# Kernel optimization log

Hardware: AMD Instinct MI355X
Metric: run time of the kernel (lower is better)

The kernel has to match this reference:

```python
import jax, jax.numpy as jnp
import numpy as np


def setup_inputs() -> dict:
    key = jax.random.key(0)
    k1, k2 = jax.random.split(key)
    B, S, H, D = 4, 2048, 12, 64
    v = jax.random.normal(k1, (B, S, H, D), dtype=jnp.float32)
    # learned per-head positional weights, sorted ascending along last dim
    # (mirrors torch.sort(torch.randn(H, S), dim=-1)[0])
    w = jnp.sort(jax.random.normal(k2, (H, S), dtype=jnp.float32), axis=-1)
    return {"v": v, "w": w}


def reference(v, w):
    # PositionalBias._naive
    # v: [B, S, H, D]; w: [H, S_max]
    B, S, H, D = v.shape
    seq_len = S - 2  # v[:, 1:-1] is the non-special-token span
    w_ = w[:, :seq_len]  # [H, seq_len]
    # _construct_bias builds bias[h, l, j] = w[h, |l - j|] (symmetric Toeplitz)
    pos = jnp.arange(seq_len)
    idx = jnp.abs(pos[:, None] - pos[None, :])  # [seq_len, seq_len]
    bias = w_[:, idx]  # [H, seq_len, seq_len]
    # zero-pad one row/col on each side -> [H, S, S]
    bias = jnp.pad(bias, ((0, 0), (1, 1), (1, 1)))
    # z_pb: [1, S, H]
    z_pb = jnp.sum(bias, axis=-1).T[None, :, :]
    # pbv: [B, S, H, D]
    pbv = jnp.einsum('nlhd,hlj->njhd', v, bias)
    return (pbv, z_pb)
```

## Files before the change

kernel.cpp:

```cpp
#include <hip/hip_runtime.h>
#include <hip/hip_bf16.h>


typedef short short8 __attribute__((ext_vector_type(8)));
typedef float floatx4 __attribute__((ext_vector_type(4)));

#define TL 2280

__device__ __forceinline__ unsigned short f2bf(float f) {
  union { __hip_bfloat16 b; unsigned short u; } cv;
  cv.b = __float2bfloat16(f);
  return cv.u;
}

__global__ __launch_bounds__(256, 3) void fused_kernel(const float* __restrict__ v,
                                                       const float* __restrict__ w,
                                                       float* __restrict__ out) {
  __shared__ __attribute__((aligned(16))) short Tls[8 * TL];

  const int bx  = blockIdx.x;
  const int tid = threadIdx.x;

  if (bx >= 768) {
    const int h = bx - 768;
    float* wv  = (float*)Tls;
    float* pfx = ((float*)Tls) + 2048;
    __shared__ float wsum[4];
    const float* wh = w + (size_t)h * 2048;
    float* zout = out + 6291456;
    for (int i = tid; i < 2048; i += 256) wv[i] = (i < 2046) ? wh[i] : 0.f;
    __syncthreads();
    const int base = tid * 8;
    float run0 = 0.f;
    #pragma unroll
    for (int k = 0; k < 8; ++k) run0 += wv[base + k];
    float x = run0;
    #pragma unroll
    for (int dd = 1; dd < 64; dd <<= 1) {
      float y = __shfl_up(x, dd);
      if ((tid & 63) >= dd) x += y;
    }
    if ((tid & 63) == 63) wsum[tid >> 6] = x;
    __syncthreads();
    const int wid4 = tid >> 6;
    float woff = 0.f;
    #pragma unroll
    for (int u = 0; u < 3; ++u) { float t = wsum[u]; if (u < wid4) woff += t; }
    float pr = x + woff - run0;
    #pragma unroll
    for (int k = 0; k < 8; ++k) { pr += wv[base + k]; pfx[base + k] = pr; }
    __syncthreads();
    for (int i = tid; i < 2046; i += 256) {
      float z = pfx[i] + pfx[2045 - i] - wv[0];
      zout[(size_t)(i + 1) * 12 + h] = z;
    }
    if (tid == 0) { zout[h] = 0.f; zout[(size_t)2047 * 12 + h] = 0.f; }
    return;
  }

  const int slice = bx % 48;
  const int jt    = bx / 48;
  const int ndt = slice & 3;
  const int h   = slice >> 2;
  const int lane = tid & 63, wid = tid >> 6;
  const int lm = lane & 15, quad = lane >> 4;
  const int jb = jt * 128;
  const int d  = wid * 16 + lm;

  const float* vrow = v + (((size_t)ndt * 2048) * 12 + h) * 64 + d;

  float r0[16], rA[16];
  {
    const int lb = quad * 8;
    #pragma unroll
    for (int i = 0; i < 8; ++i) r0[i]     = vrow[(size_t)(lb + i) * 768];
    #pragma unroll
    for (int i = 0; i < 8; ++i) r0[8 + i] = vrow[(size_t)(lb + 32 + i) * 768];
    #pragma unroll
    for (int i = 0; i < 8; ++i) rA[i]     = vrow[(size_t)(64 + lb + i) * 768];
    #pragma unroll
    for (int i = 0; i < 8; ++i) rA[8 + i] = vrow[(size_t)(64 + 32 + lb + i) * 768];
  }

  const float* wh = w + (size_t)h * 2048;
  for (int g = tid; g < 8 * (TL / 8); g += 256) {
    int c  = g / (TL / 8);
    int p8 = (g - c * (TL / 8)) * 8;
    unsigned short buf[8] __attribute__((aligned(16)));
    #pragma unroll
    for (int i = 0; i < 8; ++i) {
      int t = 127 + jb - (p8 + i) - c;
      int a = t < 0 ? -t : t;
      buf[i] = (a <= 2045) ? f2bf(wh[a]) : (unsigned short)0;
    }
    *(short8*)&Tls[c * TL + p8] = *(const short8*)buf;
  }
  __syncthreads();

  const int abase = 127 + quad * 8 - lm;
  auto load_af = [&](int p) -> short8 {
    int p0 = p + abase;
    int c = p0 & 7;
    return *(const short8*)&Tls[c * TL + (p0 - c)];
  };

  auto packB = [&](const float* f, short8& b0, short8& b1) {
    #pragma unroll
    for (int i = 0; i < 8; ++i) {
      b0[i] = (short)f2bf(f[i]);
      b1[i] = (short)f2bf(f[8 + i]);
    }
  };

  short8 afr[10];
  #pragma unroll
  for (int i = 0; i < 10; ++i) afr[i] = load_af((i - 7) * 16);

  short8 bc0, bc1;
  packB(r0, bc0, bc1);
  if (quad == 0) bc0[0] = 0;

  floatx4 acc[8];
  #pragma unroll
  for (int ma = 0; ma < 8; ++ma) acc[ma] = (floatx4){0.f, 0.f, 0.f, 0.f};

  #pragma unroll
  for (int t = 0; t < 32; ++t) {
    float rN[16];
    if (t < 30) {
      const int lb2 = (t + 2) * 64 + quad * 8;
      #pragma unroll
      for (int i = 0; i < 8; ++i) rN[i]     = vrow[(size_t)(lb2 + i) * 768];
      #pragma unroll
      for (int i = 0; i < 8; ++i) rN[8 + i] = vrow[(size_t)(lb2 + 32 + i) * 768];
    }
    short8 na0, na1, na2, na3;
    if (t < 31) {
      const int l0n = t * 64 + 64;
      na0 = load_af(l0n - 16);
      na1 = load_af(l0n);
      na2 = load_af(l0n + 16);
      na3 = load_af(l0n + 32);
    }

    __builtin_amdgcn_s_setprio(1);
    #pragma unroll
    for (int ma = 0; ma < 8; ++ma)
      acc[ma] = __builtin_amdgcn_mfma_f32_16x16x32_bf16(afr[7 - ma], bc0, acc[ma], 0, 0, 0);
    #pragma unroll
    for (int ma = 0; ma < 8; ++ma)
      acc[ma] = __builtin_amdgcn_mfma_f32_16x16x32_bf16(afr[9 - ma], bc1, acc[ma], 0, 0, 0);
    __builtin_amdgcn_s_setprio(0);

    if (t < 31) {
      short8 nb0, nb1;
      packB(rA, nb0, nb1);
      if (t == 30 && quad == 3) nb1[7] = 0;
      bc0 = nb0; bc1 = nb1;
      #pragma unroll
      for (int i = 0; i < 6; ++i) afr[i] = afr[i + 4];
      afr[6] = na0; afr[7] = na1; afr[8] = na2; afr[9] = na3;
      if (t < 30) {
        #pragma unroll
        for (int i = 0; i < 16; ++i) rA[i] = rN[i];
      }
    }
  }

  float* obase = out + (size_t)ndt * 1572864 + (size_t)h * 64 + d;
  #pragma unroll
  for (int ma = 0; ma < 8; ++ma) {
    floatx4 cc = acc[ma];
    #pragma unroll
    for (int r = 0; r < 4; ++r) {
      int j = jb + ma * 16 + quad * 4 + r;
      float val = (j == 0 || j == 2047) ? 0.f : cc[r];
      obase[(size_t)j * 768] = val;
    }
  }
}

extern "C" void kernel_launch(void* const* d_in, const int* in_sizes, int n_in,
                              void* d_out, int out_size, void* d_ws, size_t ws_size,
                              hipStream_t stream) {
  const float* v = (const float*)d_in[0];
  const float* w = (const float*)d_in[1];
  float* out = (float*)d_out;
  fused_kernel<<<dim3(780), 256, 0, stream>>>(v, w, out);
}
```

Measured before the change: 120.8 us.

## Widen j-tile to 256 and split head dim across blocks with 128-thread blocks

```diff
diff --git a/kernel.cpp b/kernel.cpp
--- a/kernel.cpp
+++ b/kernel.cpp
@@ -5,7 +5,7 @@
 typedef short short8 __attribute__((ext_vector_type(8)));
 typedef float floatx4 __attribute__((ext_vector_type(4)));
 
-#define TL 2280
+#define TL 2304
 
 __device__ __forceinline__ unsigned short f2bf(float f) {
   union { __hip_bfloat16 b; unsigned short u; } cv;
@@ -13,7 +13,7 @@
   return cv.u;
 }
 
-__global__ __launch_bounds__(256, 3) void fused_kernel(const float* __restrict__ v,
+__global__ __launch_bounds__(128, 2) void fused_kernel(const float* __restrict__ v,
                                                        const float* __restrict__ w,
                                                        float* __restrict__ out) {
   __shared__ __attribute__((aligned(16))) short Tls[8 * TL];
@@ -25,15 +25,15 @@
     const int h = bx - 768;
     float* wv  = (float*)Tls;
     float* pfx = ((float*)Tls) + 2048;
-    __shared__ float wsum[4];
+    __shared__ float wsum[2];
     const float* wh = w + (size_t)h * 2048;
     float* zout = out + 6291456;
-    for (int i = tid; i < 2048; i += 256) wv[i] = (i < 2046) ? wh[i] : 0.f;
+    for (int i = tid; i < 2048; i += 128) wv[i] = (i < 2046) ? wh[i] : 0.f;
     __syncthreads();
-    const int base = tid * 8;
+    const int base = tid * 16;
     float run0 = 0.f;
     #pragma unroll
-    for (int k = 0; k < 8; ++k) run0 += wv[base + k];
+    for (int k = 0; k < 16; ++k) run0 += wv[base + k];
     float x = run0;
     #pragma unroll
     for (int dd = 1; dd < 64; dd <<= 1) {
@@ -42,15 +42,12 @@
     }
     if ((tid & 63) == 63) wsum[tid >> 6] = x;
     __syncthreads();
-    const int wid4 = tid >> 6;
-    float woff = 0.f;
-    #pragma unroll
-    for (int u = 0; u < 3; ++u) { float t = wsum[u]; if (u < wid4) woff += t; }
+    float woff = (tid >> 6) ? wsum[0] : 0.f;
     float pr = x + woff - run0;
     #pragma unroll
-    for (int k = 0; k < 8; ++k) { pr += wv[base + k]; pfx[base + k] = pr; }
+    for (int k = 0; k < 16; ++k) { pr += wv[base + k]; pfx[base + k] = pr; }
     __syncthreads();
-    for (int i = tid; i < 2046; i += 256) {
+    for (int i = tid; i < 2046; i += 128) {
       float z = pfx[i] + pfx[2045 - i] - wv[0];
       zout[(size_t)(i + 1) * 12 + h] = z;
     }
@@ -59,37 +56,35 @@
   }
 
   const int slice = bx % 48;
-  const int jt    = bx / 48;
+  const int rest  = bx / 48;
+  const int jp    = rest >> 1;
+  const int dh    = rest & 1;
   const int ndt = slice & 3;
   const int h   = slice >> 2;
   const int lane = tid & 63, wid = tid >> 6;
   const int lm = lane & 15, quad = lane >> 4;
-  const int jb = jt * 128;
-  const int d  = wid * 16 + lm;
+  const int jb = jp * 256;
+  const int d  = dh * 32 + wid * 16 + lm;
 
   const float* vrow = v + (((size_t)ndt * 2048) * 12 + h) * 64 + d;
 
-  float r0[16], rA[16];
+  float r0[16];
   {
     const int lb = quad * 8;
     #pragma unroll
     for (int i = 0; i < 8; ++i) r0[i]     = vrow[(size_t)(lb + i) * 768];
     #pragma unroll
     for (int i = 0; i < 8; ++i) r0[8 + i] = vrow[(size_t)(lb + 32 + i) * 768];
-    #pragma unroll
-    for (int i = 0; i < 8; ++i) rA[i]     = vrow[(size_t)(64 + lb + i) * 768];
-    #pragma unroll
-    for (int i = 0; i < 8; ++i) rA[8 + i] = vrow[(size_t)(64 + 32 + lb + i) * 768];
   }
 
   const float* wh = w + (size_t)h * 2048;
-  for (int g = tid; g < 8 * (TL / 8); g += 256) {
+  for (int g = tid; g < 8 * (TL / 8); g += 128) {
     int c  = g / (TL / 8);
     int p8 = (g - c * (TL / 8)) * 8;
     unsigned short buf[8] __attribute__((aligned(16)));
     #pragma unroll
     for (int i = 0; i < 8; ++i) {
-      int t = 127 + jb - (p8 + i) - c;
+      int t = 255 + jb - (p8 + i) - c;
       int a = t < 0 ? -t : t;
       buf[i] = (a <= 2045) ? f2bf(wh[a]) : (unsigned short)0;
     }
@@ -97,9 +92,9 @@
   }
   __syncthreads();
 
-  const int abase = 127 + quad * 8 - lm;
+  const int ABASE = 255 + quad * 8 - lm;
   auto load_af = [&](int p) -> short8 {
-    int p0 = p + abase;
+    int p0 = p + ABASE;
     int c = p0 & 7;
     return *(const short8*)&Tls[c * TL + (p0 - c)];
   };
@@ -112,23 +107,26 @@
     }
   };
 
-  short8 afr[10];
+  short8 afr[18];
   #pragma unroll
-  for (int i = 0; i < 10; ++i) afr[i] = load_af((i - 7) * 16);
+  for (int i = 0; i < 18; ++i) afr[i] = load_af((i - 15) * 16);
 
   short8 bc0, bc1;
   packB(r0, bc0, bc1);
   if (quad == 0) bc0[0] = 0;
 
-  floatx4 acc[8];
+  floatx4 acc0[8], acc1[8];
   #pragma unroll
-  for (int ma = 0; ma < 8; ++ma) acc[ma] = (floatx4){0.f, 0.f, 0.f, 0.f};
+  for (int ma = 0; ma < 8; ++ma) {
+    acc0[ma] = (floatx4){0.f, 0.f, 0.f, 0.f};
+    acc1[ma] = (floatx4){0.f, 0.f, 0.f, 0.f};
+  }
 
-  #pragma unroll
+  #pragma unroll 4
   for (int t = 0; t < 32; ++t) {
     float rN[16];
-    if (t < 30) {
-      const int lb2 = (t + 2) * 64 + quad * 8;
+    if (t < 31) {
+      const int lb2 = (t + 1) * 64 + quad * 8;
       #pragma unroll
       for (int i = 0; i < 8; ++i) rN[i]     = vrow[(size_t)(lb2 + i) * 768];
       #pragma unroll
@@ -146,36 +144,42 @@
     __builtin_amdgcn_s_setprio(1);
     #pragma unroll
     for (int ma = 0; ma < 8; ++ma)
-      acc[ma] = __builtin_amdgcn_mfma_f32_16x16x32_bf16(afr[7 - ma], bc0, acc[ma], 0, 0, 0);
+      acc0[ma] = __builtin_amdgcn_mfma_f32_16x16x32_bf16(afr[15 - ma], bc0, acc0[ma], 0, 0, 0);
     #pragma unroll
     for (int ma = 0; ma < 8; ++ma)
-      acc[ma] = __builtin_amdgcn_mfma_f32_16x16x32_bf16(afr[9 - ma], bc1, acc[ma], 0, 0, 0);
+      acc1[ma] = __builtin_amdgcn_mfma_f32_16x16x32_bf16(afr[7 - ma], bc0, acc1[ma], 0, 0, 0);
+    #pragma unroll
+    for (int ma = 0; ma < 8; ++ma)
+      acc0[ma] = __builtin_amdgcn_mfma_f32_16x16x32_bf16(afr[17 - ma], bc1, acc0[ma], 0, 0, 0);
+    #pragma unroll
+    for (int ma = 0; ma < 8; ++ma)
+      acc1[ma] = __builtin_amdgcn_mfma_f32_16x16x32_bf16(afr[9 - ma], bc1, acc1[ma], 0, 0, 0);
     __builtin_amdgcn_s_setprio(0);
 
     if (t < 31) {
       short8 nb0, nb1;
-      packB(rA, nb0, nb1);
+      packB(rN, nb0, nb1);
       if (t == 30 && quad == 3) nb1[7] = 0;
       bc0 = nb0; bc1 = nb1;
       #pragma unroll
-      for (int i = 0; i < 6; ++i) afr[i] = afr[i + 4];
-      afr[6] = na0; afr[7] = na1; afr[8] = na2; afr[9] = na3;
-      if (t < 30) {
-        #pragma unroll
-        for (int i = 0; i < 16; ++i) rA[i] = rN[i];
-      }
+      for (int i = 0; i < 14; ++i) afr[i] = afr[i + 4];
+      afr[14] = na0; afr[15] = na1; afr[16] = na2; afr[17] = na3;
     }
   }
 
   float* obase = out + (size_t)ndt * 1572864 + (size_t)h * 64 + d;
   #pragma unroll
   for (int ma = 0; ma < 8; ++ma) {
-    floatx4 cc = acc[ma];
+    floatx4 c0 = acc0[ma];
+    floatx4 c1 = acc1[ma];
     #pragma unroll
     for (int r = 0; r < 4; ++r) {
-      int j = jb + ma * 16 + quad * 4 + r;
-      float val = (j == 0 || j == 2047) ? 0.f : cc[r];
-      obase[(size_t)j * 768] = val;
+      int j0 = jb + ma * 16 + quad * 4 + r;
+      int j1 = j0 + 128;
+      float v0 = (j0 == 0) ? 0.f : c0[r];
+      float v1 = (j1 == 2047) ? 0.f : c1[r];
+      obase[(size_t)j0 * 768] = v0;
+      obase[(size_t)j1 * 768] = v1;
     }
   }
 }
@@ -186,5 +190,5 @@
   const float* v = (const float*)d_in[0];
   const float* w = (const float*)d_in[1];
   float* out = (float*)d_out;
-  fused_kernel<<<dim3(780), 256, 0, stream>>>(v, w, out);
+  fused_kernel<<<dim3(780), 128, 0, stream>>>(v, w, out);
 }
```

New measurement: 118.1 us. 2.2% less time.

## Precompute bf16 Toeplitz table in global memory and split into prep and GEMM kernels

Applied to the files above, without the earlier changes.

```diff
diff --git a/kernel.cpp b/kernel.cpp
--- a/kernel.cpp
+++ b/kernel.cpp
@@ -5,7 +5,9 @@
 typedef short short8 __attribute__((ext_vector_type(8)));
 typedef float floatx4 __attribute__((ext_vector_type(4)));
 
-#define TL 2280
+#define QN 4352
+
+__device__ __attribute__((aligned(16))) short g_wt[12 * QN * 8];
 
 __device__ __forceinline__ unsigned short f2bf(float f) {
   union { __hip_bfloat16 b; unsigned short u; } cv;
@@ -13,96 +15,84 @@
   return cv.u;
 }
 
-__global__ __launch_bounds__(256, 3) void fused_kernel(const float* __restrict__ v,
-                                                       const float* __restrict__ w,
-                                                       float* __restrict__ out) {
-  __shared__ __attribute__((aligned(16))) short Tls[8 * TL];
+__global__ __launch_bounds__(256) void prep_kernel(const float* __restrict__ w,
+                                                   float* __restrict__ out) {
+  __shared__ float zls[4096];
+  __shared__ float wsum[4];
 
   const int bx  = blockIdx.x;
   const int tid = threadIdx.x;
 
-  if (bx >= 768) {
-    const int h = bx - 768;
-    float* wv  = (float*)Tls;
-    float* pfx = ((float*)Tls) + 2048;
-    __shared__ float wsum[4];
+  if (bx < 12) {
+    const int h = bx;
     const float* wh = w + (size_t)h * 2048;
-    float* zout = out + 6291456;
-    for (int i = tid; i < 2048; i += 256) wv[i] = (i < 2046) ? wh[i] : 0.f;
-    __syncthreads();
-    const int base = tid * 8;
-    float run0 = 0.f;
-    #pragma unroll
-    for (int k = 0; k < 8; ++k) run0 += wv[base + k];
-    float x = run0;
-    #pragma unroll
-    for (int dd = 1; dd < 64; dd <<= 1) {
-      float y = __shfl_up(x, dd);
-      if ((tid & 63) >= dd) x += y;
+    short* F = g_wt + (size_t)h * QN * 8;
+    for (int q = tid; q < QN; q += 256) {
+      unsigned short buf[8] __attribute__((aligned(16)));
+      #pragma unroll
+      for (int i = 0; i < 8; ++i) {
+        int t = 2174 - q - i;
+        int a = t < 0 ? -t : t;
+        buf[i] = (a <= 2045) ? f2bf(wh[a]) : (unsigned short)0;
+      }
+      *(short8*)&F[(size_t)q * 8] = *(const short8*)buf;
     }
-    if ((tid & 63) == 63) wsum[tid >> 6] = x;
-    __syncthreads();
-    const int wid4 = tid >> 6;
-    float woff = 0.f;
-    #pragma unroll
-    for (int u = 0; u < 3; ++u) { float t = wsum[u]; if (u < wid4) woff += t; }
-    float pr = x + woff - run0;
-    #pragma unroll
-    for (int k = 0; k < 8; ++k) { pr += wv[base + k]; pfx[base + k] = pr; }
-    __syncthreads();
-    for (int i = tid; i < 2046; i += 256) {
-      float z = pfx[i] + pfx[2045 - i] - wv[0];
-      zout[(size_t)(i + 1) * 12 + h] = z;
-    }
-    if (tid == 0) { zout[h] = 0.f; zout[(size_t)2047 * 12 + h] = 0.f; }
     return;
   }
 
-  const int slice = bx % 48;
-  const int jt    = bx / 48;
-  const int ndt = slice & 3;
-  const int h   = slice >> 2;
-  const int lane = tid & 63, wid = tid >> 6;
+  const int h = bx - 12;
+  float* wvv = zls;
+  float* pfx = zls + 2048;
+  const float* wh = w + (size_t)h * 2048;
+  float* zout = out + 6291456;
+  for (int i = tid; i < 2048; i += 256) wvv[i] = (i < 2046) ? wh[i] : 0.f;
+  __syncthreads();
+  const int base = tid * 8;
+  float run0 = 0.f;
+  #pragma unroll
+  for (int k = 0; k < 8; ++k) run0 += wvv[base + k];
+  float x = run0;
+  #pragma unroll
+  for (int dd = 1; dd < 64; dd <<= 1) {
+    float y = __shfl_up(x, dd);
+    if ((tid & 63) >= dd) x += y;
+  }
+  if ((tid & 63) == 63) wsum[tid >> 6] = x;
+  __syncthreads();
+  const int wid4 = tid >> 6;
+  float woff = 0.f;
+  #pragma unroll
+  for (int u = 0; u < 3; ++u) { float t = wsum[u]; if (u < wid4) woff += t; }
+  float pr = x + woff - run0;
+  #pragma unroll
+  for (int k = 0; k < 8; ++k) { pr += wvv[base + k]; pfx[base + k] = pr; }
+  __syncthreads();
+  for (int i = tid; i < 2046; i += 256) {
+    float z = pfx[i] + pfx[2045 - i] - wvv[0];
+    zout[(size_t)(i + 1) * 12 + h] = z;
+  }
+  if (tid == 0) { zout[h] = 0.f; zout[(size_t)2047 * 12 + h] = 0.f; }
+}
+
+__global__ __launch_bounds__(64, 4) void gemm_kernel(const float* __restrict__ v,
+                                                     float* __restrict__ out) {
+  const int bx   = blockIdx.x;
+  const int lane = threadIdx.x;
+
+  const int slice = bx % 192;
+  const int jt    = bx / 192;
+  const int ndq   = slice & 3;
+  const int sl    = slice >> 2;
+  const int n = sl & 3;
+  const int h = sl >> 2;
   const int lm = lane & 15, quad = lane >> 4;
   const int jb = jt * 128;
-  const int d  = wid * 16 + lm;
+  const int d  = ndq * 16 + lm;
 
-  const float* vrow = v + (((size_t)ndt * 2048) * 12 + h) * 64 + d;
+  const float* vrow = v + (((size_t)n * 2048) * 12 + h) * 64 + d;
 
-  float r0[16], rA[16];
-  {
-    const int lb = quad * 8;
-    #pragma unroll
-    for (int i = 0; i < 8; ++i) r0[i]     = vrow[(size_t)(lb + i) * 768];
-    #pragma unroll
-    for (int i = 0; i < 8; ++i) r0[8 + i] = vrow[(size_t)(lb + 32 + i) * 768];
-    #pragma unroll
-    for (int i = 0; i < 8; ++i) rA[i]     = vrow[(size_t)(64 + lb + i) * 768];
-    #pragma unroll
-    for (int i = 0; i < 8; ++i) rA[8 + i] = vrow[(size_t)(64 + 32 + lb + i) * 768];
-  }
-
-  const float* wh = w + (size_t)h * 2048;
-  for (int g = tid; g < 8 * (TL / 8); g += 256) {
-    int c  = g / (TL / 8);
-    int p8 = (g - c * (TL / 8)) * 8;
-    unsigned short buf[8] __attribute__((aligned(16)));
-    #pragma unroll
-    for (int i = 0; i < 8; ++i) {
-      int t = 127 + jb - (p8 + i) - c;
-      int a = t < 0 ? -t : t;
-      buf[i] = (a <= 2045) ? f2bf(wh[a]) : (unsigned short)0;
-    }
-    *(short8*)&Tls[c * TL + p8] = *(const short8*)buf;
-  }
-  __syncthreads();
-
-  const int abase = 127 + quad * 8 - lm;
-  auto load_af = [&](int p) -> short8 {
-    int p0 = p + abase;
-    int c = p0 & 7;
-    return *(const short8*)&Tls[c * TL + (p0 - c)];
-  };
+  const int qbase = 127 + quad * 8 - lm + 2047 - jb;
+  const short* wtb = g_wt + (size_t)h * QN * 8 + (size_t)qbase * 8;
 
   auto packB = [&](const float* f, short8& b0, short8& b1) {
     #pragma unroll
@@ -112,10 +102,14 @@
     }
   };
 
-  short8 afr[10];
-  #pragma unroll
-  for (int i = 0; i < 10; ++i) afr[i] = load_af((i - 7) * 16);
-
+  float r0[16];
+  {
+    const int lb = quad * 8;
+    #pragma unroll
+    for (int i = 0; i < 8; ++i) r0[i]     = vrow[(size_t)(lb + i) * 768];
+    #pragma unroll
+    for (int i = 0; i < 8; ++i) r0[8 + i] = vrow[(size_t)(lb + 32 + i) * 768];
+  }
   short8 bc0, bc1;
   packB(r0, bc0, bc1);
   if (quad == 0) bc0[0] = 0;
@@ -124,50 +118,41 @@
   #pragma unroll
   for (int ma = 0; ma < 8; ++ma) acc[ma] = (floatx4){0.f, 0.f, 0.f, 0.f};
 
-  #pragma unroll
+  #pragma unroll 4
   for (int t = 0; t < 32; ++t) {
+    const short* wp = wtb + (size_t)t * 512;
+    short8 af[10];
+    #pragma unroll
+    for (int gi = 0; gi < 10; ++gi)
+      af[gi] = *(const short8*)&wp[(gi - 7) * 128];
+
     float rN[16];
-    if (t < 30) {
-      const int lb2 = (t + 2) * 64 + quad * 8;
+    if (t < 31) {
+      const int lb2 = (t + 1) * 64 + quad * 8;
       #pragma unroll
       for (int i = 0; i < 8; ++i) rN[i]     = vrow[(size_t)(lb2 + i) * 768];
       #pragma unroll
       for (int i = 0; i < 8; ++i) rN[8 + i] = vrow[(size_t)(lb2 + 32 + i) * 768];
     }
-    short8 na0, na1, na2, na3;
-    if (t < 31) {
-      const int l0n = t * 64 + 64;
-      na0 = load_af(l0n - 16);
-      na1 = load_af(l0n);
-      na2 = load_af(l0n + 16);
-      na3 = load_af(l0n + 32);
-    }
 
     __builtin_amdgcn_s_setprio(1);
     #pragma unroll
     for (int ma = 0; ma < 8; ++ma)
-      acc[ma] = __builtin_amdgcn_mfma_f32_16x16x32_bf16(afr[7 - ma], bc0, acc[ma], 0, 0, 0);
+      acc[ma] = __builtin_amdgcn_mfma_f32_16x16x32_bf16(af[7 - ma], bc0, acc[ma], 0, 0, 0);
     #pragma unroll
     for (int ma = 0; ma < 8; ++ma)
-      acc[ma] = __builtin_amdgcn_mfma_f32_16x16x32_bf16(afr[9 - ma], bc1, acc[ma], 0, 0, 0);
+      acc[ma] = __builtin_amdgcn_mfma_f32_16x16x32_bf16(af[9 - ma], bc1, acc[ma], 0, 0, 0);
     __builtin_amdgcn_s_setprio(0);
 
     if (t < 31) {
       short8 nb0, nb1;
-      packB(rA, nb0, nb1);
+      packB(rN, nb0, nb1);
       if (t == 30 && quad == 3) nb1[7] = 0;
       bc0 = nb0; bc1 = nb1;
-      #pragma unroll
-      for (int i = 0; i < 6; ++i) afr[i] = afr[i + 4];
-      afr[6] = na0; afr[7] = na1; afr[8] = na2; afr[9] = na3;
-      if (t < 30) {
-        #pragma unroll
-        for (int i = 0; i < 16; ++i) rA[i] = rN[i];
-      }
     }
   }
 
-  float* obase = out + (size_t)ndt * 1572864 + (size_t)h * 64 + d;
+  float* obase = out + (size_t)n * 1572864 + (size_t)h * 64 + d;
   #pragma unroll
   for (int ma = 0; ma < 8; ++ma) {
     floatx4 cc = acc[ma];
@@ -186,5 +171,6 @@
   const float* v = (const float*)d_in[0];
   const float* w = (const float*)d_in[1];
   float* out = (float*)d_out;
-  fused_kernel<<<dim3(780), 256, 0, stream>>>(v, w, out);
+  prep_kernel<<<dim3(24), 256, 0, stream>>>(w, out);
+  gemm_kernel<<<dim3(3072), 64, 0, stream>>>(v, out);
 }
```

After: 150.4 us. 1.24x slower.
